# Kernel tuning notes

Hardware: AMD Instinct MI355X
Metric: run time of the kernel (lower is better)

The kernel has to match this reference:

```python
import jax, jax.numpy as jnp
import numpy as np

EMB = 1024
HEADS = 16
HEAD_DIM = EMB // HEADS


def setup_inputs() -> dict:
    key = jax.random.key(0)
    ks = jax.random.split(key, 6)
    B, S = 4, 1024
    inputs = jax.random.normal(ks[0], (B, S, EMB), dtype=jnp.float32)
    # causal mask: 1.0 where attention is disallowed (added * -1e9 in the layer)
    mask = (1.0 - jnp.tril(jnp.ones((S, S), dtype=jnp.float32)))[None, None, :, :]
    scale = 1.0 / np.sqrt(EMB)
    wq = jax.random.normal(ks[1], (EMB, EMB), dtype=jnp.float32) * scale
    wk = jax.random.normal(ks[2], (EMB, EMB), dtype=jnp.float32) * scale
    wv = jax.random.normal(ks[3], (EMB, EMB), dtype=jnp.float32) * scale
    wo = jax.random.normal(ks[4], (EMB, EMB), dtype=jnp.float32) * scale
    zb = jnp.zeros((EMB,), dtype=jnp.float32)
    return {"inputs": inputs, "mask": mask, "wq": wq, "bq": zb, "wk": wk,
            "bk": zb, "wv": wv, "bv": zb, "wo": wo, "bo": zb}


def _split_heads(t, B):
    # [B, S, E] -> [B, H, S, Dh]
    return t.reshape(B, -1, HEADS, HEAD_DIM).transpose(0, 2, 1, 3)


def reference(inputs, mask, wq, bq, wk, bk, wv, bv, wo, bo):
    B = inputs.shape[0]
    q = _split_heads(inputs @ wq + bq, B)
    k = _split_heads(inputs @ wk + bk, B)
    v = _split_heads(inputs @ wv + bv, B)
    # NOTE: source divides by sqrt(sqrt(head_num)) = head_num**0.25
    scores = jnp.einsum('bhsd,bhtd->bhst', q, k) / jnp.asarray(HEADS, inputs.dtype) ** 0.25
    if mask is not None:
        scores = scores + mask * -1e9
    attn = jax.nn.softmax(scores, axis=-1)
    z = jnp.einsum('bhst,bhtd->bhsd', attn, v)
    # Faithful to source: reshape [B,H,S,Dh] -> [B,S,E] WITHOUT transposing heads back
    z = z.reshape(B, -1, EMB)
    return z @ wo + bo
```

## Files before the change

### kernel.cpp

```cpp
#include <hip/hip_runtime.h>
#include <hip/hip_bf16.h>
#include <stdint.h>

typedef __attribute__((ext_vector_type(8))) short short8;
typedef __attribute__((ext_vector_type(4))) float float4v;

#define SEQ   1024
#define NQKV  3072

__device__ __forceinline__ float bf2f(ushort h) {
    union { uint u; float f; } c; c.u = ((uint)h) << 16; return c.f;
}
__device__ __forceinline__ ushort f2bf(float f) {
    union { uint u; float f; } c; c.f = f;
    uint u = c.u;
    return (ushort)((u + 0x7fffu + ((u >> 16) & 1u)) >> 16);
}
__device__ __forceinline__ void gl2lds16(const ushort* g, ushort* l) {
    __builtin_amdgcn_global_load_lds(
        (const __attribute__((address_space(1))) unsigned int*)(g),
        (__attribute__((address_space(3))) unsigned int*)(l),
        16, 0, 0);
}

__global__ void detect_k(const uint* __restrict__ x, int* __restrict__ flag) {
    __shared__ int cnt[256];
    int h = 0;
    for (int i = threadIdx.x; i < 4096; i += 256) {
        uint w = x[i];
        uint e = (w >> 7) & 0xFFu;
        h += (e >= 100u && e <= 130u) ? 1 : 0;
    }
    cnt[threadIdx.x] = h;
    __syncthreads();
    if (threadIdx.x == 0) {
        int s = 0;
        for (int i = 0; i < 256; i++) s += cnt[i];
        flag[0] = (s > 2048) ? 0 : 1;
    }
}

__global__ __launch_bounds__(256) void xcvt_k(const void* __restrict__ x,
                                              ushort* __restrict__ xc,
                                              const int* __restrict__ flag) {
    if (!*flag) return;
    int i = (blockIdx.x * 256 + threadIdx.x) * 4;
    const float* xf = (const float*)x;
    float4 v = *(const float4*)(xf + i);
    ushort4 o;
    o.x = f2bf(v.x); o.y = f2bf(v.y); o.z = f2bf(v.z); o.w = f2bf(v.w);
    *(ushort4*)(xc + i) = o;
}

__global__ void biascat_k(const void* __restrict__ bq, const void* __restrict__ bk,
                          const void* __restrict__ bv, const void* __restrict__ bo,
                          const int* __restrict__ flag, ushort* __restrict__ bout) {
    int i = blockIdx.x * 256 + threadIdx.x;
    int sel = i >> 10, j = i & 1023;
    const void* p = (sel == 0) ? bq : (sel == 1) ? bk : (sel == 2) ? bv : bo;
    bout[i] = (*flag) ? f2bf(((const float*)p)[j]) : ((const ushort*)p)[j];
}

__global__ __launch_bounds__(256) void transpose4_k(const void* __restrict__ w0,
                                                    const void* __restrict__ w1,
                                                    const void* __restrict__ w2,
                                                    const void* __restrict__ w3,
                                                    ushort* __restrict__ outall,
                                                    const int* __restrict__ flag) {
    __shared__ ushort tile[64][72];
    int z = blockIdx.z;
    const void* in = (z == 0) ? w0 : (z == 1) ? w1 : (z == 2) ? w2 : w3;
    ushort* out = outall + (size_t)z * 1024 * 1024;
    int k0 = blockIdx.x * 64;
    int n0 = blockIdx.y * 64;
    int t = threadIdx.x;
    int r = t >> 3, c = (t & 7) * 8;
    bool isf = (*flag != 0);
#pragma unroll
    for (int p = 0; p < 2; p++) {
        int rr = r + p * 32;
        if (isf) {
            const float* src = (const float*)in + (size_t)(k0 + rr) * 1024 + n0 + c;
            float4 v0 = *(const float4*)src;
            float4 v1 = *(const float4*)(src + 4);
            tile[rr][c + 0] = f2bf(v0.x); tile[rr][c + 1] = f2bf(v0.y);
            tile[rr][c + 2] = f2bf(v0.z); tile[rr][c + 3] = f2bf(v0.w);
            tile[rr][c + 4] = f2bf(v1.x); tile[rr][c + 5] = f2bf(v1.y);
            tile[rr][c + 6] = f2bf(v1.z); tile[rr][c + 7] = f2bf(v1.w);
        } else {
            uint4 v = *(const uint4*)((const ushort*)in + (size_t)(k0 + rr) * 1024 + n0 + c);
            *(uint4*)&tile[rr][c] = v;
        }
    }
    __syncthreads();
#pragma unroll
    for (int p = 0; p < 2; p++) {
        int n = r + p * 32;
        ushort vals[8];
#pragma unroll
        for (int j = 0; j < 8; j++) vals[j] = tile[c + j][n];
        *(uint4*)(out + (size_t)(n0 + n) * 1024 + k0 + c) = *(uint4*)vals;
    }
}

__global__ __launch_bounds__(256) void vtrans_k(const ushort* __restrict__ qkv,
                                                ushort* __restrict__ vt) {
    __shared__ ushort tile[64][72];
    int t0 = blockIdx.x * 64;
    int bh = blockIdx.y;
    int b = bh >> 4, h = bh & 15;
    int t = threadIdx.x;
    int r = t >> 3, c = (t & 7) * 8;
#pragma unroll
    for (int p = 0; p < 2; p++) {
        int rr = r + p * 32;
        uint4 v = *(const uint4*)(qkv + (size_t)(b * 1024 + t0 + rr) * NQKV + 2048 + h * 64 + c);
        *(uint4*)&tile[rr][c] = v;
    }
    __syncthreads();
#pragma unroll
    for (int p = 0; p < 2; p++) {
        int d = r + p * 32;
        ushort vals[8];
#pragma unroll
        for (int j = 0; j < 8; j++) vals[j] = tile[c + j][d];
        *(uint4*)(vt + ((size_t)bh * 64 + d) * 1024 + t0 + c) = *(uint4*)vals;
    }
}

template <int BM, bool DUAL>
__global__ __launch_bounds__(256) void gemm_k(const ushort* __restrict__ Araw,
                                              const ushort* __restrict__ Aconv,
                                              const ushort* __restrict__ BT,
                                              const ushort* __restrict__ bias,
                                              void* __restrict__ C,
                                              const int* __restrict__ flag,
                                              int M, int N, int K) {
    constexpr int RM = BM / 32;
    __shared__ ushort As[BM * 32];
    __shared__ ushort Bs[128 * 32];
    int n0 = blockIdx.x * 128, m0 = blockIdx.y * BM;
    int t = threadIdx.x;
    int w = t >> 6, lane = t & 63, q = lane >> 4, ln = lane & 15;
    int wr = w >> 1, wc = w & 1;
    const ushort* A = (*flag) ? Aconv : Araw;

    float4v acc[RM][4];
#pragma unroll
    for (int r = 0; r < RM; r++)
#pragma unroll
        for (int cc = 0; cc < 4; cc++) acc[r][cc] = (float4v){0.f, 0.f, 0.f, 0.f};

    for (int k0 = 0; k0 < K; k0 += 32) {
#pragma unroll
        for (int j = 0; j < BM / 64; j++) {
            int c = j * 256 + t;
            int row = c >> 2, s = c & 3;
            int kc = s ^ ((row >> 1) & 3);
            gl2lds16(A + (size_t)(m0 + row) * K + k0 + kc * 8, &As[c * 8]);
        }
#pragma unroll
        for (int j = 0; j < 2; j++) {
            int c = j * 256 + t;
            int row = c >> 2, s = c & 3;
            int kc = s ^ ((row >> 1) & 3);
            gl2lds16(BT + (size_t)(n0 + row) * K + k0 + kc * 8, &Bs[c * 8]);
        }
        __syncthreads();
        short8 af[RM], bf[4];
#pragma unroll
        for (int r = 0; r < RM; r++) {
            int row = wr * (BM / 2) + r * 16 + ln;
            af[r] = *(const short8*)&As[((row << 2) | (q ^ ((row >> 1) & 3))) * 8];
        }
#pragma unroll
        for (int cc = 0; cc < 4; cc++) {
            int col = wc * 64 + cc * 16 + ln;
            bf[cc] = *(const short8*)&Bs[((col << 2) | (q ^ ((col >> 1) & 3))) * 8];
        }
#pragma unroll
        for (int r = 0; r < RM; r++)
#pragma unroll
            for (int cc = 0; cc < 4; cc++)
                acc[r][cc] = __builtin_amdgcn_mfma_f32_16x16x32_bf16(af[r], bf[cc], acc[r][cc], 0, 0, 0);
        __syncthreads();
    }

    bool outf = DUAL && (*flag != 0);
#pragma unroll
    for (int cc = 0; cc < 4; cc++) {
        int n = n0 + wc * 64 + cc * 16 + ln;
        float bs = bf2f(bias[n]);
#pragma unroll
        for (int r = 0; r < RM; r++) {
#pragma unroll
            for (int i = 0; i < 4; i++) {
                int m = m0 + wr * (BM / 2) + r * 16 + q * 4 + i;
                float v = acc[r][cc][i] + bs;
                if (outf) ((float*)C)[(size_t)m * N + n] = v;
                else      ((ushort*)C)[(size_t)m * N + n] = f2bf(v);
            }
        }
    }
}

__global__ __launch_bounds__(512) void attn_k(const ushort* __restrict__ qkv,
                                              const ushort* __restrict__ vt,
                                              ushort* __restrict__ zp) {
    __shared__ ushort Ks[2][64 * 64];
    __shared__ ushort Vs[2][64 * 64];
    __shared__ ushort P[8][16 * 76];
    int pr = blockIdx.x;
    int bh = blockIdx.y;
    int b = bh >> 4, h = bh & 15;
    int t = threadIdx.x;
    int w = t >> 6;
    int grp = w >> 2;
    int lane = t & 63, q = lane >> 4, ln = lane & 15;

    const float CE = 0.72134752f;

    const ushort* Qp = qkv + (size_t)(b * SEQ) * NQKV + h * 64;
    const ushort* Kp = qkv + (size_t)(b * SEQ) * NQKV + 1024 + h * 64;
    const ushort* Vt = vt + (size_t)bh * 64 * 1024;

    int row0 = t >> 3, kc0 = (t & 7) ^ (row0 & 7);

    int tiB = 15 - pr;
    int ti = grp ? tiB : pr;
    int sw = ti * 64 + (w & 3) * 16;

    short8 aq0 = *(const short8*)(Qp + (size_t)(sw + ln) * NQKV + q * 8);
    short8 aq1 = *(const short8*)(Qp + (size_t)(sw + ln) * NQKV + 32 + q * 8);

    float lp[4];
    float4v o[4];
#pragma unroll
    for (int i = 0; i < 4; i++) lp[i] = 0.f;
#pragma unroll
    for (int nb = 0; nb < 4; nb++) o[nb] = (float4v){0.f, 0.f, 0.f, 0.f};

    gl2lds16(Kp + (size_t)row0 * NQKV + kc0 * 8, &Ks[0][t * 8]);
    gl2lds16(Vt + (size_t)row0 * 1024 + kc0 * 8, &Vs[0][t * 8]);

    for (int kt = 0; kt <= tiB; kt++) {
        int cur = kt & 1;
        int t0 = kt * 64;
        __syncthreads();
        if (kt < tiB) {
            int nt0 = t0 + 64, nxt = cur ^ 1;
            gl2lds16(Kp + (size_t)(nt0 + row0) * NQKV + kc0 * 8, &Ks[nxt][t * 8]);
            gl2lds16(Vt + (size_t)row0 * 1024 + nt0 + kc0 * 8, &Vs[nxt][t * 8]);
        }
        if (kt <= ti) {
            float4v s[4];
#pragma unroll
            for (int nb = 0; nb < 4; nb++) {
                int row = nb * 16 + ln;
                short8 kf0 = *(const short8*)&Ks[cur][((row << 3) | (q ^ (row & 7))) * 8];
                short8 kf1 = *(const short8*)&Ks[cur][((row << 3) | ((4 + q) ^ (row & 7))) * 8];
                s[nb] = (float4v){0.f, 0.f, 0.f, 0.f};
                s[nb] = __builtin_amdgcn_mfma_f32_16x16x32_bf16(aq0, kf0, s[nb], 0, 0, 0);
                s[nb] = __builtin_amdgcn_mfma_f32_16x16x32_bf16(aq1, kf1, s[nb], 0, 0, 0);
            }
            float p[4][4];
            if (kt < ti) {
#pragma unroll
                for (int nb = 0; nb < 4; nb++)
#pragma unroll
                    for (int i = 0; i < 4; i++) p[nb][i] = exp2f(s[nb][i] * CE);
            } else {
#pragma unroll
                for (int nb = 0; nb < 4; nb++)
#pragma unroll
                    for (int i = 0; i < 4; i++) {
                        int srow = sw + q * 4 + i;
                        int col = t0 + nb * 16 + ln;
                        p[nb][i] = exp2f((col <= srow) ? s[nb][i] * CE : -1e30f);
                    }
            }
#pragma unroll
            for (int i = 0; i < 4; i++)
                lp[i] += (p[0][i] + p[1][i]) + (p[2][i] + p[3][i]);
#pragma unroll
            for (int nb = 0; nb < 4; nb++)
#pragma unroll
                for (int i = 0; i < 4; i++)
                    P[w][(q * 4 + i) * 76 + nb * 16 + ln] = f2bf(p[nb][i]);
            asm volatile("s_waitcnt lgkmcnt(0)\n" ::: "memory");
            short8 ap0 = *(const short8*)&P[w][ln * 76 + q * 8];
            short8 ap1 = *(const short8*)&P[w][ln * 76 + 32 + q * 8];
#pragma unroll
            for (int nb = 0; nb < 4; nb++) {
                int row = nb * 16 + ln;
                short8 bv0 = *(const short8*)&Vs[cur][((row << 3) | (q ^ (row & 7))) * 8];
                short8 bv1 = *(const short8*)&Vs[cur][((row << 3) | ((4 + q) ^ (row & 7))) * 8];
                o[nb] = __builtin_amdgcn_mfma_f32_16x16x32_bf16(ap0, bv0, o[nb], 0, 0, 0);
                o[nb] = __builtin_amdgcn_mfma_f32_16x16x32_bf16(ap1, bv1, o[nb], 0, 0, 0);
            }
        }
    }

    float l_i[4];
#pragma unroll
    for (int i = 0; i < 4; i++) {
        float s = lp[i];
#pragma unroll
        for (int mk = 1; mk < 16; mk <<= 1) s += __shfl_xor(s, mk, 64);
        l_i[i] = s;
    }
#pragma unroll
    for (int nb = 0; nb < 4; nb++) {
#pragma unroll
        for (int i = 0; i < 4; i++) {
            int srow = sw + q * 4 + i;
            int d = nb * 16 + ln;
            float z = o[nb][i] / l_i[i];
            int sp = h * 64 + (srow >> 4);
            int ep = ((srow & 15) << 6) + d;
            zp[((size_t)(b * SEQ + sp)) * 1024 + ep] = f2bf(z);
        }
    }
}

extern "C" void kernel_launch(void* const* d_in, const int* in_sizes, int n_in,
                              void* d_out, int out_size, void* d_ws, size_t ws_size,
                              hipStream_t stream) {
    const void* X  = d_in[0];
    const void* wq = d_in[2];
    const void* bq = d_in[3];
    const void* wk = d_in[4];
    const void* bk = d_in[5];
    const void* wv = d_in[6];
    const void* bv = d_in[7];
    const void* wo = d_in[8];
    const void* bo = d_in[9];

    char* ws = (char*)d_ws;
    int*    flag  = (int*)ws;
    ushort* biasq = (ushort*)(ws + 4096);
    ushort* WTall = (ushort*)(ws + 12288);
    ushort* Xc    = (ushort*)(ws + 8400896);
    ushort* QKV   = (ushort*)(ws + 16789504);
    ushort* VT    = (ushort*)(ws + 41955328);
    ushort* WTo   = WTall + 3 * 1024 * 1024;
    ushort* ZP    = Xc;

    detect_k<<<1, 256, 0, stream>>>((const uint*)X, flag);
    xcvt_k<<<4096, 256, 0, stream>>>(X, Xc, flag);
    biascat_k<<<16, 256, 0, stream>>>(bq, bk, bv, bo, flag, biasq);
    transpose4_k<<<dim3(16, 16, 4), 256, 0, stream>>>(wq, wk, wv, wo, WTall, flag);
    gemm_k<128, false><<<dim3(24, 32), 256, 0, stream>>>(
        (const ushort*)X, Xc, WTall, biasq, QKV, flag, 4096, NQKV, 1024);
    vtrans_k<<<dim3(16, 64), 256, 0, stream>>>(QKV, VT);
    attn_k<<<dim3(8, 64), 512, 0, stream>>>(QKV, VT, ZP);
    gemm_k<64, true><<<dim3(8, 64), 256, 0, stream>>>(
        ZP, ZP, WTo, biasq + 3072, d_out, flag, 4096, 1024, 1024);
}
```

Before: 199.3 us.

## Fuse prep kernels into one launch and double GEMM K-tile to 64

Merges the dtype-detect, input conversion, bias concat and weight transpose kernels into a single prep kernel. Every block now redoes a cheap ballot-based dtype check on 256 words, which removes three launches and the serial dependency on the detect kernel. Separately, the GEMM K-step grows from 32 to 64 with an 8-way XOR swizzle, halving the number of barrier pairs per tile at the cost of doubled LDS use. The detection sample and threshold change from 4096 words with a >2048 count to 256 words with a >128 count, which could classify inputs differently in edge cases.

```diff
diff --git a/kernel.cpp b/kernel.cpp
--- a/kernel.cpp
+++ b/kernel.cpp
@@ -23,83 +23,79 @@
         16, 0, 0);
 }
 
-__global__ void detect_k(const uint* __restrict__ x, int* __restrict__ flag) {
-    __shared__ int cnt[256];
-    int h = 0;
-    for (int i = threadIdx.x; i < 4096; i += 256) {
-        uint w = x[i];
-        uint e = (w >> 7) & 0xFFu;
-        h += (e >= 100u && e <= 130u) ? 1 : 0;
-    }
-    cnt[threadIdx.x] = h;
+__global__ __launch_bounds__(256) void prep_k(const void* __restrict__ X,
+                                              const void* __restrict__ w0,
+                                              const void* __restrict__ w1,
+                                              const void* __restrict__ w2,
+                                              const void* __restrict__ w3,
+                                              const void* __restrict__ bq,
+                                              const void* __restrict__ bk,
+                                              const void* __restrict__ bv,
+                                              const void* __restrict__ bo,
+                                              ushort* __restrict__ xc,
+                                              ushort* __restrict__ biasout,
+                                              ushort* __restrict__ wtall,
+                                              int* __restrict__ flag) {
+    __shared__ int tot;
+    __shared__ ushort tile[64][72];
+    int t = threadIdx.x;
+    if (t == 0) tot = 0;
     __syncthreads();
-    if (threadIdx.x == 0) {
-        int s = 0;
-        for (int i = 0; i < 256; i++) s += cnt[i];
-        flag[0] = (s > 2048) ? 0 : 1;
-    }
-}
-
-__global__ __launch_bounds__(256) void xcvt_k(const void* __restrict__ x,
-                                              ushort* __restrict__ xc,
-                                              const int* __restrict__ flag) {
-    if (!*flag) return;
-    int i = (blockIdx.x * 256 + threadIdx.x) * 4;
-    const float* xf = (const float*)x;
-    float4 v = *(const float4*)(xf + i);
-    ushort4 o;
-    o.x = f2bf(v.x); o.y = f2bf(v.y); o.z = f2bf(v.z); o.w = f2bf(v.w);
-    *(ushort4*)(xc + i) = o;
-}
-
-__global__ void biascat_k(const void* __restrict__ bq, const void* __restrict__ bk,
-                          const void* __restrict__ bv, const void* __restrict__ bo,
-                          const int* __restrict__ flag, ushort* __restrict__ bout) {
-    int i = blockIdx.x * 256 + threadIdx.x;
-    int sel = i >> 10, j = i & 1023;
-    const void* p = (sel == 0) ? bq : (sel == 1) ? bk : (sel == 2) ? bv : bo;
-    bout[i] = (*flag) ? f2bf(((const float*)p)[j]) : ((const ushort*)p)[j];
-}
-
-__global__ __launch_bounds__(256) void transpose4_k(const void* __restrict__ w0,
-                                                    const void* __restrict__ w1,
-                                                    const void* __restrict__ w2,
-                                                    const void* __restrict__ w3,
-                                                    ushort* __restrict__ outall,
-                                                    const int* __restrict__ flag) {
-    __shared__ ushort tile[64][72];
-    int z = blockIdx.z;
-    const void* in = (z == 0) ? w0 : (z == 1) ? w1 : (z == 2) ? w2 : w3;
-    ushort* out = outall + (size_t)z * 1024 * 1024;
-    int k0 = blockIdx.x * 64;
-    int n0 = blockIdx.y * 64;
-    int t = threadIdx.x;
-    int r = t >> 3, c = (t & 7) * 8;
-    bool isf = (*flag != 0);
-#pragma unroll
-    for (int p = 0; p < 2; p++) {
-        int rr = r + p * 32;
-        if (isf) {
-            const float* src = (const float*)in + (size_t)(k0 + rr) * 1024 + n0 + c;
-            float4 v0 = *(const float4*)src;
-            float4 v1 = *(const float4*)(src + 4);
-            tile[rr][c + 0] = f2bf(v0.x); tile[rr][c + 1] = f2bf(v0.y);
-            tile[rr][c + 2] = f2bf(v0.z); tile[rr][c + 3] = f2bf(v0.w);
-            tile[rr][c + 4] = f2bf(v1.x); tile[rr][c + 5] = f2bf(v1.y);
-            tile[rr][c + 6] = f2bf(v1.z); tile[rr][c + 7] = f2bf(v1.w);
-        } else {
-            uint4 v = *(const uint4*)((const ushort*)in + (size_t)(k0 + rr) * 1024 + n0 + c);
-            *(uint4*)&tile[rr][c] = v;
-        }
-    }
+    uint wv = ((const uint*)X)[t];
+    uint e = (wv >> 7) & 0xFFu;
+    bool isbf = (e >= 100u && e <= 130u);
+    unsigned long long m = __ballot(isbf);
+    if ((t & 63) == 0) atomicAdd(&tot, __popcll(m));
     __syncthreads();
-#pragma unroll
-    for (int p = 0; p < 2; p++) {
-        int n = r + p * 32;
-        ushort vals[8];
-#pragma unroll
-        for (int j = 0; j < 8; j++) vals[j] = tile[c + j][n];
-        *(uint4*)(out + (size_t)(n0 + n) * 1024 + k0 + c) = *(uint4*)vals;
+    bool isf = (tot <= 128);
+
+    int bi = blockIdx.x;
+    if (bi == 0 && t == 0) flag[0] = isf ? 1 : 0;
+
+    if (bi < 4096) {
+        if (!isf) return;
+        int i = (bi * 256 + t) * 4;
+        float4 v = *(const float4*)((const float*)X + i);
+        ushort4 o;
+        o.x = f2bf(v.x); o.y = f2bf(v.y); o.z = f2bf(v.z); o.w = f2bf(v.w);
+        *(ushort4*)(xc + i) = o;
+    } else if (bi < 4112) {
+        int i = (bi - 4096) * 256 + t;
+        int sel = i >> 10, j = i & 1023;
+        const void* p = (sel == 0) ? bq : (sel == 1) ? bk : (sel == 2) ? bv : bo;
+        biasout[i] = isf ? f2bf(((const float*)p)[j]) : ((const ushort*)p)[j];
+    } else {
+        int idx = bi - 4112;
+        int z = idx >> 8, rem = idx & 255;
+        const void* in = (z == 0) ? w0 : (z == 1) ? w1 : (z == 2) ? w2 : w3;
+        ushort* out = wtall + (size_t)z * 1024 * 1024;
+        int k0 = (rem & 15) * 64, n0 = (rem >> 4) * 64;
+        int r = t >> 3, c = (t & 7) * 8;
+#pragma unroll
+        for (int p = 0; p < 2; p++) {
+            int rr = r + p * 32;
+            if (isf) {
+                const float* src = (const float*)in + (size_t)(k0 + rr) * 1024 + n0 + c;
+                float4 v0 = *(const float4*)src;
+                float4 v1 = *(const float4*)(src + 4);
+                tile[rr][c + 0] = f2bf(v0.x); tile[rr][c + 1] = f2bf(v0.y);
+                tile[rr][c + 2] = f2bf(v0.z); tile[rr][c + 3] = f2bf(v0.w);
+                tile[rr][c + 4] = f2bf(v1.x); tile[rr][c + 5] = f2bf(v1.y);
+                tile[rr][c + 6] = f2bf(v1.z); tile[rr][c + 7] = f2bf(v1.w);
+            } else {
+                uint4 v = *(const uint4*)((const ushort*)in + (size_t)(k0 + rr) * 1024 + n0 + c);
+                *(uint4*)&tile[rr][c] = v;
+            }
+        }
+        __syncthreads();
+#pragma unroll
+        for (int p = 0; p < 2; p++) {
+            int n = r + p * 32;
+            ushort vals[8];
+#pragma unroll
+            for (int j = 0; j < 8; j++) vals[j] = tile[c + j][n];
+            *(uint4*)(out + (size_t)(n0 + n) * 1024 + k0 + c) = *(uint4*)vals;
+        }
     }
 }
 
@@ -137,8 +133,8 @@
                                               const int* __restrict__ flag,
                                               int M, int N, int K) {
     constexpr int RM = BM / 32;
-    __shared__ ushort As[BM * 32];
-    __shared__ ushort Bs[128 * 32];
+    __shared__ ushort As[BM * 64];
+    __shared__ ushort Bs[128 * 64];
     int n0 = blockIdx.x * 128, m0 = blockIdx.y * BM;
     int t = threadIdx.x;
     int w = t >> 6, lane = t & 63, q = lane >> 4, ln = lane & 15;
@@ -151,38 +147,42 @@
 #pragma unroll
         for (int cc = 0; cc < 4; cc++) acc[r][cc] = (float4v){0.f, 0.f, 0.f, 0.f};
 
-    for (int k0 = 0; k0 < K; k0 += 32) {
-#pragma unroll
-        for (int j = 0; j < BM / 64; j++) {
+    for (int k0 = 0; k0 < K; k0 += 64) {
+#pragma unroll
+        for (int j = 0; j < RM; j++) {
             int c = j * 256 + t;
-            int row = c >> 2, s = c & 3;
-            int kc = s ^ ((row >> 1) & 3);
+            int row = c >> 3, s = c & 7;
+            int kc = s ^ (row & 7);
             gl2lds16(A + (size_t)(m0 + row) * K + k0 + kc * 8, &As[c * 8]);
         }
 #pragma unroll
-        for (int j = 0; j < 2; j++) {
+        for (int j = 0; j < 4; j++) {
             int c = j * 256 + t;
-            int row = c >> 2, s = c & 3;
-            int kc = s ^ ((row >> 1) & 3);
+            int row = c >> 3, s = c & 7;
+            int kc = s ^ (row & 7);
             gl2lds16(BT + (size_t)(n0 + row) * K + k0 + kc * 8, &Bs[c * 8]);
         }
         __syncthreads();
-        short8 af[RM], bf[4];
-#pragma unroll
-        for (int r = 0; r < RM; r++) {
-            int row = wr * (BM / 2) + r * 16 + ln;
-            af[r] = *(const short8*)&As[((row << 2) | (q ^ ((row >> 1) & 3))) * 8];
-        }
-#pragma unroll
-        for (int cc = 0; cc < 4; cc++) {
-            int col = wc * 64 + cc * 16 + ln;
-            bf[cc] = *(const short8*)&Bs[((col << 2) | (q ^ ((col >> 1) & 3))) * 8];
-        }
-#pragma unroll
-        for (int r = 0; r < RM; r++)
-#pragma unroll
-            for (int cc = 0; cc < 4; cc++)
-                acc[r][cc] = __builtin_amdgcn_mfma_f32_16x16x32_bf16(af[r], bf[cc], acc[r][cc], 0, 0, 0);
+#pragma unroll
+        for (int half = 0; half < 2; half++) {
+            int qc = half * 4 + q;
+            short8 af[RM], bf[4];
+#pragma unroll
+            for (int r = 0; r < RM; r++) {
+                int row = wr * (BM / 2) + r * 16 + ln;
+                af[r] = *(const short8*)&As[((row << 3) | (qc ^ (row & 7))) * 8];
+            }
+#pragma unroll
+            for (int cc = 0; cc < 4; cc++) {
+                int col = wc * 64 + cc * 16 + ln;
+                bf[cc] = *(const short8*)&Bs[((col << 3) | (qc ^ (col & 7))) * 8];
+            }
+#pragma unroll
+            for (int r = 0; r < RM; r++)
+#pragma unroll
+                for (int cc = 0; cc < 4; cc++)
+                    acc[r][cc] = __builtin_amdgcn_mfma_f32_16x16x32_bf16(af[r], bf[cc], acc[r][cc], 0, 0, 0);
+        }
         __syncthreads();
     }
 
@@ -346,10 +346,8 @@
     ushort* WTo   = WTall + 3 * 1024 * 1024;
     ushort* ZP    = Xc;
 
-    detect_k<<<1, 256, 0, stream>>>((const uint*)X, flag);
-    xcvt_k<<<4096, 256, 0, stream>>>(X, Xc, flag);
-    biascat_k<<<16, 256, 0, stream>>>(bq, bk, bv, bo, flag, biasq);
-    transpose4_k<<<dim3(16, 16, 4), 256, 0, stream>>>(wq, wk, wv, wo, WTall, flag);
+    prep_k<<<5136, 256, 0, stream>>>(X, wq, wk, wv, wo, bq, bk, bv, bo,
+                                     Xc, biasq, WTall, flag);
     gemm_k<128, false><<<dim3(24, 32), 256, 0, stream>>>(
         (const ushort*)X, Xc, WTall, biasq, QKV, flag, 4096, NQKV, 1024);
     vtrans_k<<<dim3(16, 64), 256, 0, stream>>>(QKV, VT);
```

New measurement: 196.9 us. No clear change (-1.2%).
